# Kernel tuning notes

Measured on AMD Instinct MI355X. Metric: run time of the kernel, lower is better.

The kernel has to match this reference:

```python
import jax, jax.numpy as jnp
import numpy as np

B, T, S_ENC, H, V = 8, 128, 400, 256, 50257


def setup_inputs() -> dict:
    key = jax.random.key(0)
    ks = jax.random.split(key, 16)
    inp = {
        "input_tokens": jax.random.randint(ks[0], (B, S_ENC), 0, V),
        "context": jax.random.normal(ks[1], (B, T, H), dtype=jnp.float32),
        "decoder_input": jax.random.normal(ks[2], (B, T, H), dtype=jnp.float32),
        "decoder_output": jax.random.normal(ks[3], (B, T, H), dtype=jnp.float32),
        "vocab_dist": jax.random.uniform(ks[4], (B, T, V), dtype=jnp.float32),
        "attn_dist": jax.random.uniform(ks[5], (B, T, S_ENC), dtype=jnp.float32),
        "encoder_outputs": jax.random.normal(ks[6], (B, S_ENC, H), dtype=jnp.float32),
        # Linear(H, 1) params for the three p_gen projections
        "Wc": jax.random.normal(ks[7], (H, 1), dtype=jnp.float32) / np.sqrt(H),
        "bc": jnp.zeros((1,), dtype=jnp.float32),
        "Wo": jax.random.normal(ks[8], (H, 1), dtype=jnp.float32) / np.sqrt(H),
        "bo": jnp.zeros((1,), dtype=jnp.float32),
        "Wi": jax.random.normal(ks[9], (H, 1), dtype=jnp.float32) / np.sqrt(H),
        "bi": jnp.zeros((1,), dtype=jnp.float32),
    }
    return inp


def reference(input_tokens, context, decoder_input, decoder_output, vocab_dist,
              attn_dist, encoder_outputs, Wc, bc, Wo, bo, Wi, bi):
    # p_gen: sigmoid of sum of three Linear(H,1) projections -> [B, T, 1]
    p_gen = jax.nn.sigmoid(
        context @ Wc + bc + decoder_output @ Wo + bo + decoder_input @ Wi + bi
    )
    # copy distribution: scatter_add attn_dist into a [B, T, V] zeros tensor
    # along the vocab axis at the source token ids (broadcast over T).
    b_idx = jnp.arange(vocab_dist.shape[0])[:, None, None]   # [B,1,1]
    t_idx = jnp.arange(vocab_dist.shape[1])[None, :, None]   # [1,T,1]
    copy_dist = jnp.zeros_like(vocab_dist).at[
        b_idx, t_idx, input_tokens[:, None, :]
    ].add(attn_dist)
    # gated mix (same math as torch source: vocab_dist * p_gen + (1-p_gen) * log_softmax(copy))
    final_dist = vocab_dist * p_gen + (1.0 - p_gen) * jax.nn.log_softmax(copy_dist, axis=2)
    return final_dist
```

## Files before the change

kernel.cpp:

```cpp
#include <hip/hip_runtime.h>
#include <math.h>

#define B 8
#define T 128
#define S_ENC 400
#define H 256
#define V 50257

__global__ __launch_bounds__(256) void prep_kernel(
    const int*   __restrict__ tokens,
    const float* __restrict__ context,
    const float* __restrict__ dec_in,
    const float* __restrict__ dec_out,
    const float* __restrict__ attn,
    const float* __restrict__ Wc, const float* __restrict__ bc,
    const float* __restrict__ Wo, const float* __restrict__ bo,
    const float* __restrict__ Wi, const float* __restrict__ bi,
    float4* __restrict__ params)
{
    __shared__ int           tok_s[S_ENC];
    __shared__ float         acc[S_ENC];
    __shared__ unsigned char isf[S_ENC];
    __shared__ float s_pg[4];
    __shared__ float s_m[4];
    __shared__ int   s_n[4];
    __shared__ float s_se[4];
    __shared__ float s_mb;

    const int bt   = blockIdx.x;
    const int b    = bt >> 7;
    const int tid  = threadIdx.x;
    const int lane = tid & 63;
    const int wave = tid >> 6;

    for (int s = tid; s < S_ENC; s += 256) {
        tok_s[s] = tokens[b * S_ENC + s];
        acc[s]   = 0.0f;
    }
    __syncthreads();

    {
        float v = context[bt * H + tid] * Wc[tid]
                + dec_out[bt * H + tid] * Wo[tid]
                + dec_in [bt * H + tid] * Wi[tid];
        #pragma unroll
        for (int off = 32; off; off >>= 1) v += __shfl_down(v, off, 64);
        if (lane == 0) s_pg[wave] = v;
    }

    for (int s = tid; s < S_ENC; s += 256) {
        int tk = tok_s[s];
        int f  = s;
        for (int j = 0; j < s; ++j) {
            if (tok_s[j] == tk) { f = j; break; }
        }
        isf[s] = (unsigned char)(f == s);
        atomicAdd(&acc[f], attn[bt * S_ENC + s]);
    }
    __syncthreads();

    {
        float m = 0.0f;
        int   n = 0;
        for (int s = tid; s < S_ENC; s += 256) {
            if (isf[s]) { m = fmaxf(m, acc[s]); n++; }
        }
        #pragma unroll
        for (int off = 32; off; off >>= 1) {
            m  = fmaxf(m, __shfl_down(m, off, 64));
            n += __shfl_down(n, off, 64);
        }
        if (lane == 0) { s_m[wave] = m; s_n[wave] = n; }
    }
    __syncthreads();
    if (tid == 0) {
        s_mb = fmaxf(fmaxf(s_m[0], s_m[1]), fmaxf(s_m[2], s_m[3]));
    }
    __syncthreads();

    {
        const float m = s_mb;
        float se = 0.0f;
        for (int s = tid; s < S_ENC; s += 256) {
            if (isf[s]) se += expf(acc[s] - m);
        }
        #pragma unroll
        for (int off = 32; off; off >>= 1) se += __shfl_down(se, off, 64);
        if (lane == 0) s_se[wave] = se;
    }
    __syncthreads();

    if (tid == 0) {
        const float m   = s_mb;
        const int   nnz = s_n[0] + s_n[1] + s_n[2] + s_n[3];
        float se  = s_se[0] + s_se[1] + s_se[2] + s_se[3]
                  + (float)(V - nnz) * expf(-m);
        float lse = m + logf(se);
        float x   = s_pg[0] + s_pg[1] + s_pg[2] + s_pg[3]
                  + bc[0] + bo[0] + bi[0];
        float p   = 1.0f / (1.0f + expf(-x));
        float q   = 1.0f - p;
        params[bt] = make_float4(p, q * lse, q, 0.0f);
    }
}

__global__ __launch_bounds__(256) void mix_kernel(
    const float4* __restrict__ vocab,
    const float4* __restrict__ params,
    float4* __restrict__ out)
{
    const int idx = blockIdx.x * 256 + threadIdx.x;
    const int e   = idx * 4;
    const int bt  = e / V;
    const int rem = e - bt * V;

    float4 v = vocab[idx];
    float4 o;
    if (rem + 4 <= V) {
        const float4 P = params[bt];
        o.x = v.x * P.x - P.y;
        o.y = v.y * P.x - P.y;
        o.z = v.z * P.x - P.y;
        o.w = v.w * P.x - P.y;
    } else {
        const float* vp = (const float*)&v;
        float* op = (float*)&o;
        #pragma unroll
        for (int j = 0; j < 4; ++j) {
            int btj = (e + j) / V;
            float4 P = params[btj];
            op[j] = vp[j] * P.x - P.y;
        }
    }
    out[idx] = o;
}

__global__ __launch_bounds__(256) void scatter_kernel(
    const int*   __restrict__ tokens,
    const float* __restrict__ attn,
    const float4* __restrict__ params,
    float* __restrict__ out)
{
    const int idx = blockIdx.x * 256 + threadIdx.x;
    const int bt  = idx / S_ENC;
    const int s   = idx - bt * S_ENC;
    const int b   = bt >> 7;
    const int tok = tokens[b * S_ENC + s];
    const float g = params[bt].z;
    atomicAdd(out + (size_t)bt * V + tok, g * attn[idx]);
}

extern "C" void kernel_launch(void* const* d_in, const int* in_sizes, int n_in,
                              void* d_out, int out_size, void* d_ws, size_t ws_size,
                              hipStream_t stream) {
    const int*   tokens  = (const int*)  d_in[0];
    const float* context = (const float*)d_in[1];
    const float* dec_in  = (const float*)d_in[2];
    const float* dec_out = (const float*)d_in[3];
    const float* vocab   = (const float*)d_in[4];
    const float* attn    = (const float*)d_in[5];
    const float* Wc = (const float*)d_in[7];
    const float* bc = (const float*)d_in[8];
    const float* Wo = (const float*)d_in[9];
    const float* bo = (const float*)d_in[10];
    const float* Wi = (const float*)d_in[11];
    const float* bi = (const float*)d_in[12];

    float*  out    = (float*) d_out;
    float4* params = (float4*)d_ws;

    prep_kernel<<<B * T, 256, 0, stream>>>(tokens, context, dec_in, dec_out,
                                           attn, Wc, bc, Wo, bo, Wi, bi, params);

    const int total4 = (B * T * V) / 4;
    mix_kernel<<<total4 / 256, 256, 0, stream>>>(
        (const float4*)vocab, (const float4*)params, (float4*)out);

    scatter_kernel<<<(B * T * S_ENC) / 256, 256, 0, stream>>>(
        tokens, attn, params, out);
}
```

Measured before the change: 447.0 us.

## Replace quadratic duplicate-token scan with shared hash table; use nontemporal mix loads/stores

The prep kernel drops its O(S^2) linear search for the first occurrence of each token and instead accumulates attention weights per unique token in a 1024-entry open-addressing hash table in shared memory, built with atomicCAS. The max and sum-exp reductions now scan the hash slots. Separately, the streaming mix kernel uses ext_vector float4 with nontemporal loads and stores so that vocab and output data bypass cache retention. The hash adds CAS contention and probing, and the reductions scan 1024 slots instead of 400.

```diff
diff --git a/kernel.cpp b/kernel.cpp
--- a/kernel.cpp
+++ b/kernel.cpp
@@ -6,6 +6,9 @@
 #define S_ENC 400
 #define H 256
 #define V 50257
+#define HASH_SZ 1024
+
+typedef float vfloat4 __attribute__((ext_vector_type(4)));
 
 __global__ __launch_bounds__(256) void prep_kernel(
     const int*   __restrict__ tokens,
@@ -18,9 +21,8 @@
     const float* __restrict__ Wi, const float* __restrict__ bi,
     float4* __restrict__ params)
 {
-    __shared__ int           tok_s[S_ENC];
-    __shared__ float         acc[S_ENC];
-    __shared__ unsigned char isf[S_ENC];
+    __shared__ int   hkey[HASH_SZ];
+    __shared__ float hval[HASH_SZ];
     __shared__ float s_pg[4];
     __shared__ float s_m[4];
     __shared__ int   s_n[4];
@@ -33,9 +35,10 @@
     const int lane = tid & 63;
     const int wave = tid >> 6;
 
-    for (int s = tid; s < S_ENC; s += 256) {
-        tok_s[s] = tokens[b * S_ENC + s];
-        acc[s]   = 0.0f;
+    #pragma unroll
+    for (int i = tid; i < HASH_SZ; i += 256) {
+        hkey[i] = -1;
+        hval[i] = 0.0f;
     }
     __syncthreads();
 
@@ -49,21 +52,23 @@
     }
 
     for (int s = tid; s < S_ENC; s += 256) {
-        int tk = tok_s[s];
-        int f  = s;
-        for (int j = 0; j < s; ++j) {
-            if (tok_s[j] == tk) { f = j; break; }
+        const int   tk = tokens[b * S_ENC + s];
+        const float a  = attn[bt * S_ENC + s];
+        unsigned h = ((unsigned)tk * 2654435761u >> 16) & (HASH_SZ - 1);
+        for (;;) {
+            int prev = atomicCAS(&hkey[h], -1, tk);
+            if (prev == -1 || prev == tk) { atomicAdd(&hval[h], a); break; }
+            h = (h + 1) & (HASH_SZ - 1);
         }
-        isf[s] = (unsigned char)(f == s);
-        atomicAdd(&acc[f], attn[bt * S_ENC + s]);
     }
     __syncthreads();
 
     {
         float m = 0.0f;
         int   n = 0;
-        for (int s = tid; s < S_ENC; s += 256) {
-            if (isf[s]) { m = fmaxf(m, acc[s]); n++; }
+        #pragma unroll
+        for (int i = tid; i < HASH_SZ; i += 256) {
+            if (hkey[i] != -1) { m = fmaxf(m, hval[i]); n++; }
         }
         #pragma unroll
         for (int off = 32; off; off >>= 1) {
@@ -73,16 +78,15 @@
         if (lane == 0) { s_m[wave] = m; s_n[wave] = n; }
     }
     __syncthreads();
-    if (tid == 0) {
-        s_mb = fmaxf(fmaxf(s_m[0], s_m[1]), fmaxf(s_m[2], s_m[3]));
-    }
+    if (tid == 0) s_mb = fmaxf(fmaxf(s_m[0], s_m[1]), fmaxf(s_m[2], s_m[3]));
     __syncthreads();
 
     {
         const float m = s_mb;
         float se = 0.0f;
-        for (int s = tid; s < S_ENC; s += 256) {
-            if (isf[s]) se += expf(acc[s] - m);
+        #pragma unroll
+        for (int i = tid; i < HASH_SZ; i += 256) {
+            if (hkey[i] != -1) se += expf(hval[i] - m);
         }
         #pragma unroll
         for (int off = 32; off; off >>= 1) se += __shfl_down(se, off, 64);
@@ -105,34 +109,29 @@
 }
 
 __global__ __launch_bounds__(256) void mix_kernel(
-    const float4* __restrict__ vocab,
-    const float4* __restrict__ params,
-    float4* __restrict__ out)
+    const vfloat4* __restrict__ vocab,
+    const float4*  __restrict__ params,
+    vfloat4* __restrict__ out)
 {
     const int idx = blockIdx.x * 256 + threadIdx.x;
     const int e   = idx * 4;
     const int bt  = e / V;
     const int rem = e - bt * V;
 
-    float4 v = vocab[idx];
-    float4 o;
+    vfloat4 v = __builtin_nontemporal_load(&vocab[idx]);
+    vfloat4 o;
     if (rem + 4 <= V) {
         const float4 P = params[bt];
-        o.x = v.x * P.x - P.y;
-        o.y = v.y * P.x - P.y;
-        o.z = v.z * P.x - P.y;
-        o.w = v.w * P.x - P.y;
+        o = v * P.x - P.y;
     } else {
-        const float* vp = (const float*)&v;
-        float* op = (float*)&o;
         #pragma unroll
         for (int j = 0; j < 4; ++j) {
             int btj = (e + j) / V;
             float4 P = params[btj];
-            op[j] = vp[j] * P.x - P.y;
+            o[j] = v[j] * P.x - P.y;
         }
     }
-    out[idx] = o;
+    __builtin_nontemporal_store(o, &out[idx]);
 }
 
 __global__ __launch_bounds__(256) void scatter_kernel(
@@ -174,7 +173,7 @@
 
     const int total4 = (B * T * V) / 4;
     mix_kernel<<<total4 / 256, 256, 0, stream>>>(
-        (const float4*)vocab, (const float4*)params, (float4*)out);
+        (const vfloat4*)vocab, (const float4*)params, (vfloat4*)out);
 
     scatter_kernel<<<(B * T * S_ENC) / 256, 256, 0, stream>>>(
         tokens, attn, params, out);
```

New measurement: 406.9 us. 9.0% less time.
